# Kernel tuning notes

Measured on AMD Instinct MI355X. Metric: run time of the kernel, lower is better.

Reference implementation:

```python
import jax, jax.numpy as jnp
import numpy as np

D_MODEL = 1024
NUM_HEADS = 16
ROPE_BASE = 10000.0


def _rope_sincos(T, head_dim, dtype):
    # angles[t, i] = t / base**(2i/head_dim), i in [0, head_dim//2)
    pos = jnp.arange(T, dtype=jnp.float32)[:, None]              # [T, 1]
    inv_freq = 1.0 / (ROPE_BASE ** (jnp.arange(0, head_dim, 2, dtype=jnp.float32) / head_dim))
    angles = pos * inv_freq                                       # [T, half]
    sin = jnp.sin(angles).astype(dtype)[None, :, None, :]         # [1, T, 1, half]
    cos = jnp.cos(angles).astype(dtype)[None, :, None, :]
    return sin, cos


def _apply_rope(x, sin, cos):
    # x: [B, T, H, head_dim]; deinterleave even/odd lanes, rotate, concat halves
    x1, x2 = x[..., ::2], x[..., 1::2]                            # [B, T, H, half] each
    return jnp.concatenate([x1 * cos - x2 * sin, x1 * sin + x2 * cos], axis=-1)


def setup_inputs() -> dict:
    key = jax.random.key(0)
    ks = jax.random.split(key, 5)
    B, T, D = 2, 2048, D_MODEL
    s = 0.02
    return {
        "x": jax.random.normal(ks[0], (B, T, D), dtype=jnp.float32),
        "w_qkv": jax.random.normal(ks[1], (3 * D, D), dtype=jnp.float32) * s,
        "b_qkv": jnp.zeros((3 * D,), dtype=jnp.float32),
        "w_out": jax.random.normal(ks[2], (D, D), dtype=jnp.float32) * s,
        "b_out": jnp.zeros((D,), dtype=jnp.float32),
    }


def reference(x, w_qkv, b_qkv, w_out, b_out):
    B, T, D = x.shape
    H = NUM_HEADS
    hd = D // H
    scale = hd ** -0.5

    qkv = (x @ w_qkv.T + b_qkv).reshape(B, T, 3, H, hd)
    q, k, v = qkv[:, :, 0], qkv[:, :, 1], qkv[:, :, 2]            # [B, T, H, hd]

    sin, cos = _rope_sincos(T, hd, x.dtype)
    q = _apply_rope(q, sin, cos)
    k = _apply_rope(k, sin, cos)

    scores = jnp.einsum("bthd,bshd->bhts", q, k) * scale          # [B, H, T, T]
    weights = jax.nn.softmax(scores, axis=-1)
    out = jnp.einsum("bhts,bshd->bthd", weights, v)               # [B, T, H, hd]
    out = out.reshape(B, T, D)
    return out @ w_out.T + b_out
```

## Files before the change

### kernel.cpp

```cpp
#include <hip/hip_runtime.h>
#include <cstdint>
#include <cstddef>

typedef __attribute__((ext_vector_type(8))) short short8;
typedef __attribute__((ext_vector_type(8))) __bf16 bf16x8;
typedef __attribute__((ext_vector_type(4))) float f32x4;
typedef __attribute__((ext_vector_type(16))) float f32x16;
typedef __attribute__((ext_vector_type(4))) unsigned int uint32x4;

#define LOG2E 1.44269504088896340736f

__device__ __forceinline__ unsigned short f2bf(float f) {
    unsigned int u = __builtin_bit_cast(unsigned int, f);
    u += 0x7fffu + ((u >> 16) & 1u);
    return (unsigned short)(u >> 16);
}

__device__ __forceinline__ f32x4 zero4() {
    f32x4 z; z.x = 0.f; z.y = 0.f; z.z = 0.f; z.w = 0.f; return z;
}
__device__ __forceinline__ f32x16 zero16() {
    f32x16 z;
    #pragma unroll
    for (int i = 0; i < 16; ++i) z[i] = 0.f;
    return z;
}

__device__ __forceinline__ f32x4 mfma16(short8 a, short8 b, f32x4 c) {
    return __builtin_amdgcn_mfma_f32_16x16x32_bf16(
        __builtin_bit_cast(bf16x8, a), __builtin_bit_cast(bf16x8, b), c, 0, 0, 0);
}
__device__ __forceinline__ f32x16 mfma32(short8 a, short8 b, f32x16 c) {
    return __builtin_amdgcn_mfma_f32_32x32x16_bf16(
        __builtin_bit_cast(bf16x8, a), __builtin_bit_cast(bf16x8, b), c, 0, 0, 0);
}

__device__ __forceinline__ unsigned int cvt_pk_bf16(float lo, float hi) {
    unsigned int r;
    asm("v_cvt_pk_bf16_f32 %0, %1, %2" : "=v"(r) : "v"(lo), "v"(hi));
    return r;
}

__device__ __forceinline__ uint2 permswap(unsigned x, unsigned y) {
#if __has_builtin(__builtin_amdgcn_permlane32_swap)
    auto r = __builtin_amdgcn_permlane32_swap(x, y, false, false);
    return make_uint2(r[0], r[1]);
#else
    int lane = threadIdx.x & 63;
    unsigned sy = __shfl_xor(y, 32), sx = __shfl_xor(x, 32);
    return make_uint2((lane < 32) ? x : sy, (lane < 32) ? sx : y);
#endif
}
__device__ __forceinline__ float red_max32(float v) {
    unsigned u = __builtin_bit_cast(unsigned, v);
    uint2 p = permswap(u, u);
    return fmaxf(__builtin_bit_cast(float, p.x), __builtin_bit_cast(float, p.y));
}
__device__ __forceinline__ float red_add32(float v) {
    unsigned u = __builtin_bit_cast(unsigned, v);
    uint2 p = permswap(u, u);
    return __builtin_bit_cast(float, p.x) + __builtin_bit_cast(float, p.y);
}

__device__ __forceinline__ void gload_lds16(const void* g, void* l, int lane) {
#if __has_builtin(__builtin_amdgcn_global_load_lds)
    __builtin_amdgcn_global_load_lds(
        (const __attribute__((address_space(1))) void*)g,
        (__attribute__((address_space(3))) void*)l, 16, 0, 0);
    (void)lane;
#else
    reinterpret_cast<int4*>(l)[lane] = *reinterpret_cast<const int4*>(g);
#endif
}

__global__ __launch_bounds__(256) void prep_kernel(
    const float* __restrict__ x, const float* __restrict__ wq,
    const float* __restrict__ wo,
    unsigned short* __restrict__ xb, unsigned short* __restrict__ wqb,
    unsigned short* __restrict__ wob, float2* __restrict__ tab) {
    const int S0 = 1048576, S1 = 786432, S2 = 262144;
    int i = blockIdx.x * 256 + threadIdx.x;
    const float* src; unsigned short* dst; int j;
    if (i < S0) { src = x; dst = xb; j = i; }
    else if (i < S0 + S1) { src = wq; dst = wqb; j = i - S0; }
    else if (i < S0 + S1 + S2) { src = wo; dst = wob; j = i - S0 - S1; }
    else {
        int idx = i - (S0 + S1 + S2);
        if (idx < 2048 * 32) {
            int t = idx >> 5, ii = idx & 31;
            float inv_freq = powf(10000.0f, -(float)ii / 32.0f);
            float ang = (float)t * inv_freq;
            tab[idx] = make_float2(cosf(ang), sinf(ang));
        }
        return;
    }
    float4 v = reinterpret_cast<const float4*>(src)[j];
    ushort4 o;
    o.x = f2bf(v.x); o.y = f2bf(v.y); o.z = f2bf(v.z); o.w = f2bf(v.w);
    reinterpret_cast<ushort4*>(dst)[j] = o;
}

__device__ __forceinline__ void gemm_mainloop_128x128(
    const unsigned short* __restrict__ A, const unsigned short* __restrict__ B,
    int K, int m0, int n0, unsigned short* As, unsigned short* Bs, f32x4 acc[4][4]) {
    int tid = threadIdx.x;
    int wave = tid >> 6, lane = tid & 63;
    int wm = wave >> 1, wn = wave & 1;
    int g = lane >> 4, c = lane & 15;
    const int NS = K >> 6;

    auto stage = [&](int buf, int k0) {
        #pragma unroll
        for (int i = 0; i < 4; ++i) {
            int call = wave * 4 + i;
            int s = call * 64 + lane;
            int row = s >> 3, c8 = s & 7;
            int csw = (c8 ^ (row & 7)) << 3;
            gload_lds16(A + (size_t)(m0 + row) * K + k0 + csw,
                        (char*)As + buf * 16384 + call * 1024, lane);
            gload_lds16(B + (size_t)(n0 + row) * K + k0 + csw,
                        (char*)Bs + buf * 16384 + call * 1024, lane);
        }
    };

    stage(0, 0);

    #pragma unroll 1
    for (int t = 0; t < NS; ++t) {
        int cur = t & 1;
        asm volatile("s_waitcnt vmcnt(0) lgkmcnt(0)" ::: "memory");
        __builtin_amdgcn_s_barrier();
        __builtin_amdgcn_sched_barrier(0);
        if (t + 1 < NS) stage(cur ^ 1, (t + 1) * 64);

        const char* Ac = (const char*)As + cur * 16384;
        const char* Bc = (const char*)Bs + cur * 16384;
        #pragma unroll
        for (int kg = 0; kg < 2; ++kg) {
            short8 af[4], bfr[4];
            #pragma unroll
            for (int mt = 0; mt < 4; ++mt) {
                int row = wm * 64 + mt * 16 + c;
                af[mt] = *reinterpret_cast<const short8*>(Ac +
                    ((row * 128 + kg * 64 + g * 16) ^ ((row & 7) << 4)));
            }
            #pragma unroll
            for (int nt = 0; nt < 4; ++nt) {
                int row = wn * 64 + nt * 16 + c;
                bfr[nt] = *reinterpret_cast<const short8*>(Bc +
                    ((row * 128 + kg * 64 + g * 16) ^ ((row & 7) << 4)));
            }
            __builtin_amdgcn_s_setprio(1);
            #pragma unroll
            for (int mt = 0; mt < 4; ++mt)
                #pragma unroll
                for (int nt = 0; nt < 4; ++nt)
                    acc[mt][nt] = mfma16(af[mt], bfr[nt], acc[mt][nt]);
            __builtin_amdgcn_s_setprio(0);
        }
    }
}

__global__ __launch_bounds__(256) void qkv_gemm_kernel(
    const unsigned short* __restrict__ X, const unsigned short* __restrict__ W,
    const float* __restrict__ bias, const float2* __restrict__ tab,
    unsigned short* __restrict__ q, unsigned short* __restrict__ k,
    unsigned short* __restrict__ vt) {
    __shared__ unsigned short As[2][128 * 64];
    __shared__ unsigned short Bs[2][128 * 64];
    const int K = 1024;
    const float SCL = 0.125f * LOG2E;
    int flat = blockIdx.x + 24 * blockIdx.y;
    int swzb = (flat & 7) * 96 + (flat >> 3);
    int m0 = (swzb / 24) * 128, n0 = (swzb % 24) * 128;
    f32x4 acc[4][4];
    #pragma unroll
    for (int i = 0; i < 4; ++i)
        #pragma unroll
        for (int j = 0; j < 4; ++j) acc[i][j] = zero4();

    gemm_mainloop_128x128(X, W, K, m0, n0, &As[0][0], &Bs[0][0], acc);

    int tid = threadIdx.x;
    int wave = tid >> 6, lane = tid & 63;
    int wm = wave >> 1, wn = wave & 1;
    int g = lane >> 4, c = lane & 15;
    int mbase = m0 + wm * 64, nbase = n0 + wn * 64;
    #pragma unroll
    for (int mt = 0; mt < 4; ++mt) {
        #pragma unroll
        for (int nt = 0; nt < 4; ++nt) {
            f32x4 a = acc[mt][nt];
            int n = nbase + nt * 16 + c;
            int s = n >> 10;
            int h = (n >> 6) & 15;
            int d = n & 63;
            float bn = bias[n];
            #pragma unroll
            for (int r = 0; r < 4; ++r) {
                int m = mbase + mt * 16 + g * 4 + r;
                int bb = m >> 11, t = m & 2047;
                float val = a[r] + bn;
                float partner = __shfl_xor(val, 1);
                int bh = bb * 16 + h;
                if (s == 2) {
                    vt[((size_t)bh * 64 + d) * 2048 + t] = f2bf(val);
                } else {
                    int i2 = d >> 1;
                    float2 cs = tab[t * 32 + i2];
                    float outv; int dout;
                    if ((d & 1) == 0) { outv = val * cs.x - partner * cs.y; dout = i2; }
                    else              { outv = partner * cs.y + val * cs.x; dout = 32 + i2; }
                    if (s == 0) outv *= SCL;
                    (s == 0 ? q : k)[((size_t)bh * 2048 + t) * 64 + dout] = f2bf(outv);
                }
            }
        }
    }
}

__global__ __launch_bounds__(256) void attn_kernel(
    const unsigned short* __restrict__ Q, const unsigned short* __restrict__ Kin,
    const unsigned short* __restrict__ VT, unsigned short* __restrict__ O) {
    __shared__ unsigned short Ks[3][64 * 64];
    __shared__ unsigned short VTs[3][64 * 64];
    const int T = 2048, NT = 32;
    int flat = blockIdx.x + 16 * blockIdx.y;
    int swzb = (flat & 7) * 64 + (flat >> 3);
    int bh = swzb >> 4;
    int qt = swzb & 15;
    int tid = threadIdx.x, wave = tid >> 6, lane = tid & 63;
    int lam = lane & 31, hi = lane >> 5;
    int q = qt * 128 + wave * 32 + lam;

    const unsigned short* Qb = Q + ((size_t)bh * T + q) * 64;
    const unsigned short* Kb = Kin + (size_t)bh * T * 64;
    const unsigned short* VTb = VT + (size_t)bh * 64 * T;

    uint32x4 qtmp[4];
    #pragma unroll
    for (int c4 = 0; c4 < 4; ++c4)
        qtmp[c4] = *reinterpret_cast<const uint32x4*>(Qb + c4 * 16 + hi * 8);
    #pragma unroll
    for (int c4 = 0; c4 < 4; ++c4)
        asm volatile("" : "+v"(qtmp[c4]));
    short8 qf[4];
    #pragma unroll
    for (int c4 = 0; c4 < 4; ++c4) qf[c4] = __builtin_bit_cast(short8, qtmp[c4]);

    f32x16 o0 = zero16(), o1 = zero16();
    float m_run = -1e30f, l_run = 0.0f;
    int swz = ((lam >> 2) & 7) << 4;

    auto stage = [&](int buf, int j0) {
        #pragma unroll
        for (int i = 0; i < 2; ++i) {
            int call = wave * 2 + i;
            int s = call * 64 + lane;
            int row = s >> 3, c8 = s & 7;
            int csw = (c8 ^ ((row >> 2) & 7)) << 3;
            gload_lds16(Kb + (size_t)(j0 + row) * 64 + csw,
                        (char*)&Ks[buf][0] + call * 1024, lane);
            gload_lds16(VTb + (size_t)row * T + j0 + csw,
                        (char*)&VTs[buf][0] + call * 1024, lane);
        }
    };

    stage(0, 0);
    stage(1, 64);

    int cur = 0, stb = 2;
    #pragma unroll 1
    for (int t = 0; t < NT; ++t) {
        if (t + 1 < NT) asm volatile("s_waitcnt vmcnt(4) lgkmcnt(0)" ::: "memory");
        else            asm volatile("s_waitcnt vmcnt(0) lgkmcnt(0)" ::: "memory");
        __builtin_amdgcn_s_barrier();
        __builtin_amdgcn_sched_barrier(0);
        if (t + 2 < NT) stage(stb, (t + 2) * 64);

        const char* Kc = (const char*)&Ks[cur][0];
        const char* Vc = (const char*)&VTs[cur][0];

        f32x16 s0 = zero16(), s1 = zero16();
        __builtin_amdgcn_s_setprio(1);
        #pragma unroll
        for (int c4 = 0; c4 < 4; ++c4) {
            int col = c4 * 32 + hi * 16;
            short8 kf0 = *reinterpret_cast<const short8*>(Kc + ((lam * 128 + col) ^ swz));
            s0 = mfma32(kf0, qf[c4], s0);
            short8 kf1 = *reinterpret_cast<const short8*>(Kc + (((lam + 32) * 128 + col) ^ swz));
            s1 = mfma32(kf1, qf[c4], s1);
        }
        __builtin_amdgcn_s_setprio(0);

        float mx[16];
        #pragma unroll
        for (int r = 0; r < 16; ++r) mx[r] = fmaxf(s0[r], s1[r]);
        #pragma unroll
        for (int st = 8; st > 0; st >>= 1)
            #pragma unroll
            for (int r = 0; r < st; ++r) mx[r] = fmaxf(mx[r], mx[r + st]);
        float tmax = red_max32(mx[0]);
        if (__any(tmax - m_run > 8.0f)) {
            float mnew = fmaxf(m_run, tmax);
            float alpha = exp2f(m_run - mnew);
            m_run = mnew;
            l_run *= alpha;
            #pragma unroll
            for (int r = 0; r < 16; ++r) { o0[r] *= alpha; o1[r] *= alpha; }
        }
        float p0[16], p1[16];
        #pragma unroll
        for (int r = 0; r < 16; ++r) p0[r] = exp2f(s0[r] - m_run);
        #pragma unroll
        for (int r = 0; r < 16; ++r) p1[r] = exp2f(s1[r] - m_run);

        short8 pa[4];
        #pragma unroll
        for (int blk = 0; blk < 2; ++blk) {
            const float* p = blk ? p1 : p0;
            #pragma unroll
            for (int jt = 0; jt < 2; ++jt) {
                unsigned a0 = cvt_pk_bf16(p[jt * 8 + 0], p[jt * 8 + 1]);
                unsigned a1 = cvt_pk_bf16(p[jt * 8 + 2], p[jt * 8 + 3]);
                unsigned b0 = cvt_pk_bf16(p[jt * 8 + 4], p[jt * 8 + 5]);
                unsigned b1 = cvt_pk_bf16(p[jt * 8 + 6], p[jt * 8 + 7]);
                uint2 pr0 = permswap(a0, b0);
                uint2 pr1 = permswap(a1, b1);
                uint4 w;
                w.x = pr0.x;
                w.y = pr1.x;
                w.z = pr0.y;
                w.w = pr1.y;
                pa[blk * 2 + jt] = __builtin_bit_cast(short8, w);
            }
        }

        __builtin_amdgcn_s_setprio(1);
        #pragma unroll
        for (int jt = 0; jt < 4; ++jt) {
            int col = jt * 32 + hi * 16;
            short8 vf0 = *reinterpret_cast<const short8*>(Vc + ((lam * 128 + col) ^ swz));
            o0 = mfma32(vf0, pa[jt], o0);
            short8 vf1 = *reinterpret_cast<const short8*>(Vc + (((lam + 32) * 128 + col) ^ swz));
            o1 = mfma32(vf1, pa[jt], o1);
        }
        __builtin_amdgcn_s_setprio(0);

        float sm[16];
        #pragma unroll
        for (int r = 0; r < 16; ++r) sm[r] = p0[r] + p1[r];
        #pragma unroll
        for (int st = 8; st > 0; st >>= 1)
            #pragma unroll
            for (int r = 0; r < st; ++r) sm[r] += sm[r + st];
        l_run += red_add32(sm[0]);

        cur = (cur == 2) ? 0 : cur + 1;
        stb = (stb == 2) ? 0 : stb + 1;
    }

    float rinv = 1.0f / l_run;
    int b_ = bh >> 4, h_ = bh & 15;
    unsigned short* Orow = O + ((size_t)(b_ * 2048) + q) * 1024 + h_ * 64;
    #pragma unroll
    for (int rq = 0; rq < 4; ++rq) {
        ushort4 w0, w1;
        w0.x = f2bf(o0[rq * 4 + 0] * rinv);
        w0.y = f2bf(o0[rq * 4 + 1] * rinv);
        w0.z = f2bf(o0[rq * 4 + 2] * rinv);
        w0.w = f2bf(o0[rq * 4 + 3] * rinv);
        w1.x = f2bf(o1[rq * 4 + 0] * rinv);
        w1.y = f2bf(o1[rq * 4 + 1] * rinv);
        w1.z = f2bf(o1[rq * 4 + 2] * rinv);
        w1.w = f2bf(o1[rq * 4 + 3] * rinv);
        int d0 = rq * 8 + hi * 4;
        *reinterpret_cast<ushort4*>(Orow + d0) = w0;
        *reinterpret_cast<ushort4*>(Orow + 32 + d0) = w1;
    }
}

__global__ __launch_bounds__(256) void out_gemm_kernel(
    const unsigned short* __restrict__ Aattn, const unsigned short* __restrict__ W,
    const float* __restrict__ bias, float* __restrict__ out) {
    __shared__ unsigned short As[2][128 * 64];
    __shared__ unsigned short Bs[2][128 * 64];
    const int K = 1024, N = 1024;
    int flat = blockIdx.x + 8 * blockIdx.y;
    int swzb = (flat & 7) * 32 + (flat >> 3);
    int m0 = (swzb >> 3) * 128, n0 = (swzb & 7) * 128;
    f32x4 acc[4][4];
    #pragma unroll
    for (int i = 0; i < 4; ++i)
        #pragma unroll
        for (int j = 0; j < 4; ++j) acc[i][j] = zero4();

    gemm_mainloop_128x128(Aattn, W, K, m0, n0, &As[0][0], &Bs[0][0], acc);

    int tid = threadIdx.x;
    int wave = tid >> 6, lane = tid & 63;
    int wm = wave >> 1, wn = wave & 1;
    int g = lane >> 4, c = lane & 15;
    int mbase = m0 + wm * 64, nbase = n0 + wn * 64;
    #pragma unroll
    for (int mt = 0; mt < 4; ++mt)
        #pragma unroll
        for (int nt = 0; nt < 4; ++nt) {
            int n = nbase + nt * 16 + c;
            float bn = bias[n];
            #pragma unroll
            for (int r = 0; r < 4; ++r) {
                int m = mbase + mt * 16 + g * 4 + r;
                out[(size_t)m * N + n] = acc[mt][nt][r] + bn;
            }
        }
}

extern "C" void kernel_launch(void* const* d_in, const int* in_sizes, int n_in,
                              void* d_out, int out_size, void* d_ws, size_t ws_size,
                              hipStream_t stream) {
    (void)in_sizes; (void)n_in; (void)out_size; (void)ws_size;
    const float* x     = (const float*)d_in[0];
    const float* w_qkv = (const float*)d_in[1];
    const float* b_qkv = (const float*)d_in[2];
    const float* w_out = (const float*)d_in[3];
    const float* b_out = (const float*)d_in[4];
    float* out = (float*)d_out;

    const int B = 2, T = 2048, D = 1024;
    const int M = B * T;
    const size_t MB = 1024 * 1024;

    char* ws = (char*)d_ws;
    unsigned short* xb    = (unsigned short*)(ws);
    unsigned short* wqkvb = (unsigned short*)(ws + 8 * MB);
    unsigned short* woutb = (unsigned short*)(ws + 14 * MB);
    unsigned short* qb    = (unsigned short*)(ws + 16 * MB);
    unsigned short* kb    = (unsigned short*)(ws + 24 * MB);
    unsigned short* vtb   = (unsigned short*)(ws + 32 * MB);
    unsigned short* attnb = (unsigned short*)(ws + 40 * MB);
    float2* tab           = (float2*)(ws + 48 * MB);

    prep_kernel<<<dim3((2097152 + 65536) / 256), dim3(256), 0, stream>>>(
        x, w_qkv, w_out, xb, wqkvb, woutb, tab);
    qkv_gemm_kernel<<<dim3(3 * D / 128, M / 128), dim3(256), 0, stream>>>(xb, wqkvb, b_qkv, tab, qb, kb, vtb);
    attn_kernel<<<dim3(T / 128, B * 16), dim3(256), 0, stream>>>(qb, kb, vtb, attnb);
    out_gemm_kernel<<<dim3(D / 128, M / 128), dim3(256), 0, stream>>>(attnb, woutb, b_out, out);
}
```

Before: 171.9 us.

## Split attention KV range across two wave groups and merge partial softmax

The attention block grows to 512 threads, and two groups of four waves each process half of the key/value sequence for the same 128 queries. Partial outputs, maxima and sums are merged through shared memory at the end. The row sum is now computed with an extra MFMA against a ones vector instead of cross-lane reductions, and the K/V pipeline drops from triple to double buffering with a full vmcnt(0) wait each step. This doubles waves per query tile to hide latency, at the cost of a merge step, an extra MFMA per tile and a shallower prefetch.

```diff
diff --git a/kernel.cpp b/kernel.cpp
--- a/kernel.cpp
+++ b/kernel.cpp
@@ -55,11 +55,6 @@
     unsigned u = __builtin_bit_cast(unsigned, v);
     uint2 p = permswap(u, u);
     return fmaxf(__builtin_bit_cast(float, p.x), __builtin_bit_cast(float, p.y));
-}
-__device__ __forceinline__ float red_add32(float v) {
-    unsigned u = __builtin_bit_cast(unsigned, v);
-    uint2 p = permswap(u, u);
-    return __builtin_bit_cast(float, p.x) + __builtin_bit_cast(float, p.y);
 }
 
 __device__ __forceinline__ void gload_lds16(const void* g, void* l, int lane) {
@@ -219,19 +214,20 @@
     }
 }
 
-__global__ __launch_bounds__(256) void attn_kernel(
+__global__ __launch_bounds__(512, 4) void attn_kernel(
     const unsigned short* __restrict__ Q, const unsigned short* __restrict__ Kin,
     const unsigned short* __restrict__ VT, unsigned short* __restrict__ O) {
-    __shared__ unsigned short Ks[3][64 * 64];
-    __shared__ unsigned short VTs[3][64 * 64];
-    const int T = 2048, NT = 32;
+    __shared__ int4 smem4[65536 / 16];
+    char* smem = (char*)smem4;
+    const int T = 2048, NT = 16;
     int flat = blockIdx.x + 16 * blockIdx.y;
     int swzb = (flat & 7) * 64 + (flat >> 3);
     int bh = swzb >> 4;
     int qt = swzb & 15;
     int tid = threadIdx.x, wave = tid >> 6, lane = tid & 63;
     int lam = lane & 31, hi = lane >> 5;
-    int q = qt * 128 + wave * 32 + lam;
+    int pair = wave & 3, half = wave >> 2;
+    int q = qt * 128 + pair * 32 + lam;
 
     const unsigned short* Qb = Q + ((size_t)bh * T + q) * 64;
     const unsigned short* Kb = Kin + (size_t)bh * T * 64;
@@ -248,38 +244,44 @@
     #pragma unroll
     for (int c4 = 0; c4 < 4; ++c4) qf[c4] = __builtin_bit_cast(short8, qtmp[c4]);
 
-    f32x16 o0 = zero16(), o1 = zero16();
-    float m_run = -1e30f, l_run = 0.0f;
-    int swz = ((lam >> 2) & 7) << 4;
-
-    auto stage = [&](int buf, int j0) {
+    short8 ones;
+    #pragma unroll
+    for (int i = 0; i < 8; ++i) ones[i] = (short)0x3F80;
+
+    f32x16 o0 = zero16(), o1 = zero16(), lacc = zero16();
+    float m_run = -1e30f;
+    int swz = (lam & 7) << 4;
+
+    char* Ks0 = smem + half * 16384;
+    char* Vs0 = smem + 32768 + half * 16384;
+
+    auto stage = [&](int buf, int t) {
+        int j0 = half * 1024 + t * 64;
         #pragma unroll
         for (int i = 0; i < 2; ++i) {
-            int call = wave * 2 + i;
+            int call = pair * 2 + i;
             int s = call * 64 + lane;
             int row = s >> 3, c8 = s & 7;
-            int csw = (c8 ^ ((row >> 2) & 7)) << 3;
+            int csw = (c8 ^ (row & 7)) << 3;
             gload_lds16(Kb + (size_t)(j0 + row) * 64 + csw,
-                        (char*)&Ks[buf][0] + call * 1024, lane);
+                        Ks0 + buf * 8192 + call * 1024, lane);
             gload_lds16(VTb + (size_t)row * T + j0 + csw,
-                        (char*)&VTs[buf][0] + call * 1024, lane);
+                        Vs0 + buf * 8192 + call * 1024, lane);
         }
     };
 
     stage(0, 0);
-    stage(1, 64);
-
-    int cur = 0, stb = 2;
+
     #pragma unroll 1
     for (int t = 0; t < NT; ++t) {
-        if (t + 1 < NT) asm volatile("s_waitcnt vmcnt(4) lgkmcnt(0)" ::: "memory");
-        else            asm volatile("s_waitcnt vmcnt(0) lgkmcnt(0)" ::: "memory");
+        int cur = t & 1;
+        asm volatile("s_waitcnt vmcnt(0) lgkmcnt(0)" ::: "memory");
         __builtin_amdgcn_s_barrier();
         __builtin_amdgcn_sched_barrier(0);
-        if (t + 2 < NT) stage(stb, (t + 2) * 64);
-
-        const char* Kc = (const char*)&Ks[cur][0];
-        const char* Vc = (const char*)&VTs[cur][0];
+        if (t + 1 < NT) stage(cur ^ 1, t + 1);
+
+        const char* Kc = Ks0 + cur * 8192;
+        const char* Vc = Vs0 + cur * 8192;
 
         f32x16 s0 = zero16(), s1 = zero16();
         __builtin_amdgcn_s_setprio(1);
@@ -293,21 +295,18 @@
         }
         __builtin_amdgcn_s_setprio(0);
 
-        float mx[16];
-        #pragma unroll
-        for (int r = 0; r < 16; ++r) mx[r] = fmaxf(s0[r], s1[r]);
-        #pragma unroll
-        for (int st = 8; st > 0; st >>= 1)
-            #pragma unroll
-            for (int r = 0; r < st; ++r) mx[r] = fmaxf(mx[r], mx[r + st]);
-        float tmax = red_max32(mx[0]);
+        float tm = fmaxf(s0[0], s1[0]);
+        #pragma unroll
+        for (int r = 1; r < 16; ++r) tm = fmaxf(tm, fmaxf(s0[r], s1[r]));
+        float tmax = red_max32(tm);
         if (__any(tmax - m_run > 8.0f)) {
             float mnew = fmaxf(m_run, tmax);
             float alpha = exp2f(m_run - mnew);
             m_run = mnew;
-            l_run *= alpha;
-            #pragma unroll
-            for (int r = 0; r < 16; ++r) { o0[r] *= alpha; o1[r] *= alpha; }
+            #pragma unroll
+            for (int r = 0; r < 16; ++r) {
+                o0[r] *= alpha; o1[r] *= alpha; lacc[r] *= alpha;
+            }
         }
         float p0[16], p1[16];
         #pragma unroll
@@ -344,23 +343,38 @@
             o0 = mfma32(vf0, pa[jt], o0);
             short8 vf1 = *reinterpret_cast<const short8*>(Vc + (((lam + 32) * 128 + col) ^ swz));
             o1 = mfma32(vf1, pa[jt], o1);
+            lacc = mfma32(ones, pa[jt], lacc);
         }
         __builtin_amdgcn_s_setprio(0);
-
-        float sm[16];
-        #pragma unroll
-        for (int r = 0; r < 16; ++r) sm[r] = p0[r] + p1[r];
-        #pragma unroll
-        for (int st = 8; st > 0; st >>= 1)
-            #pragma unroll
-            for (int r = 0; r < st; ++r) sm[r] += sm[r + st];
-        l_run += red_add32(sm[0]);
-
-        cur = (cur == 2) ? 0 : cur + 1;
-        stb = (stb == 2) ? 0 : stb + 1;
-    }
-
-    float rinv = 1.0f / l_run;
+    }
+
+    float l_run = lacc[0];
+
+    __syncthreads();
+    float* pb = (float*)(smem + pair * 8704);
+    if (half) {
+        #pragma unroll
+        for (int r = 0; r < 16; ++r) {
+            pb[lane * 34 + r] = o0[r];
+            pb[lane * 34 + 16 + r] = o1[r];
+        }
+        pb[lane * 34 + 32] = m_run;
+        pb[lane * 34 + 33] = l_run;
+    }
+    __syncthreads();
+    if (half) return;
+
+    float mb = pb[lane * 34 + 32], lb = pb[lane * 34 + 33];
+    float m = fmaxf(m_run, mb);
+    float wa = exp2f(m_run - m), wb = exp2f(mb - m);
+    float l = l_run * wa + lb * wb;
+    float rinv = 1.0f / l;
+    #pragma unroll
+    for (int r = 0; r < 16; ++r) {
+        o0[r] = o0[r] * wa + pb[lane * 34 + r] * wb;
+        o1[r] = o1[r] * wa + pb[lane * 34 + 16 + r] * wb;
+    }
+
     int b_ = bh >> 4, h_ = bh & 15;
     unsigned short* Orow = O + ((size_t)(b_ * 2048) + q) * 1024 + h_ * 64;
     #pragma unroll
@@ -444,6 +458,6 @@
     prep_kernel<<<dim3((2097152 + 65536) / 256), dim3(256), 0, stream>>>(
         x, w_qkv, w_out, xb, wqkvb, woutb, tab);
     qkv_gemm_kernel<<<dim3(3 * D / 128, M / 128), dim3(256), 0, stream>>>(xb, wqkvb, b_qkv, tab, qb, kb, vtb);
-    attn_kernel<<<dim3(T / 128, B * 16), dim3(256), 0, stream>>>(qb, kb, vtb, attnb);
+    attn_kernel<<<dim3(T / 128, B * 16), dim3(512), 0, stream>>>(qb, kb, vtb, attnb);
     out_gemm_kernel<<<dim3(D / 128, M / 128), dim3(256), 0, stream>>>(attnb, woutb, b_out, out);
 }
```

Measured after the change: 173.6 us. Within noise of the previous version (+1.0%).
